# Kernel optimization log

Measured on AMD Instinct MI355X. Metric: run time of the kernel, lower is better.

## Reference

```python
import jax, jax.numpy as jnp
import numpy as np

B, T, C, H, HD = 2, 2048, 1024, 16, 64
EPS = 1e-6

def rmsnorm(x):
    return x * jax.lax.rsqrt(jnp.mean(x * x, axis=-1, keepdims=True) + EPS)

def rotary_cos_sin(seq_len, hd):
    inv_freq = 1.0 / (10000.0 ** (jnp.arange(0, hd, 2, dtype=jnp.float32) / hd))
    freqs = jnp.arange(seq_len, dtype=jnp.float32)[:, None] * inv_freq[None, :]  # [T, hd/2]
    return jnp.cos(freqs)[None, :, None, :], jnp.sin(freqs)[None, :, None, :]

def apply_rotary(x, cos, sin):
    x1, x2 = x[..., : HD // 2], x[..., HD // 2 :]
    return jnp.concatenate([x1 * cos + x2 * sin, -x1 * sin + x2 * cos], axis=-1)


def setup_inputs() -> dict:
    key = jax.random.key(0)
    ks = jax.random.split(key, 8)
    return {
        "x": jax.random.normal(ks[0], (B, T, C), jnp.float32),
        "w_qkv": jax.random.normal(ks[1], (3 * C, C), jnp.float32) * 0.02,
        "w_out": jax.random.normal(ks[2], (C, C), jnp.float32) * 0.02,
        "hyp_curvature": jax.random.uniform(ks[3], (1, H, 1, 1), jnp.float32, 0.5, 1.5),
        "w_uv": jax.random.normal(ks[4], (8 * C, C), jnp.float32) * 0.02,
        "b_uv": jnp.zeros((8 * C,), jnp.float32),
        "w_mlp_out": jax.random.normal(ks[5], (C, 4 * C), jnp.float32) * 0.02,
        "b_mlp_out": jnp.zeros((C,), jnp.float32),
    }


def reference(x, w_qkv, w_out, hyp_curvature, w_uv, b_uv, w_mlp_out, b_mlp_out):
    # --- pre-norm (euc/hyp branch uses rms_norm) ---
    h = rmsnorm(x)
    # --- QKV projection ---
    qkv = h @ w_qkv.T  # [B,T,3C]
    q, k, v = jnp.split(qkv, 3, axis=-1)
    q = q.reshape(B, T, H, HD)
    k = k.reshape(B, T, H, HD)
    v = v.reshape(B, T, H, HD)
    # --- RoPE ---
    cos, sin = rotary_cos_sin(T, HD)
    q = apply_rotary(q, cos, sin)
    k = apply_rotary(k, cos, sin)
    # [B,H,T,HD]
    q = jnp.transpose(q, (0, 2, 1, 3))
    k = jnp.transpose(k, (0, 2, 1, 3))
    v = jnp.transpose(v, (0, 2, 1, 3))
    # --- hyperbolic (Lorentz) attention ---
    kc = hyp_curvature  # [1,H,1,1], positive per-head curvature
    q0 = jnp.sqrt(kc + jnp.sum(q * q, axis=-1, keepdims=True))  # time coord [B,H,T,1]
    k0 = jnp.sqrt(kc + jnp.sum(k * k, axis=-1, keepdims=True))
    # Lorentz inner product <u,v>_L = -u0*v0 + u.v  -> [B,H,T,S]
    lorentz = jnp.einsum("bhtd,bhsd->bhts", q, k) - q0 * jnp.swapaxes(k0, -1, -2)
    dis = jnp.sqrt(kc) * jnp.arccosh(jnp.maximum(-lorentz / kc, 1.0 + EPS))
    causal = jnp.tril(jnp.ones((T, T), dtype=bool))
    scores = jnp.where(causal, -dis, -jnp.inf)  # hyp_attn_weight='neg_dis'
    attn_w = jax.nn.softmax(scores, axis=-1)
    attn = jnp.einsum("bhts,bhsd->bhtd", attn_w, v)
    attn = jnp.transpose(attn, (0, 2, 1, 3)).reshape(B, T, C)
    x = x + attn @ w_out.T
    # --- SwiGLU MLP with pre rms_norm ---
    h = rmsnorm(x)
    uv = h @ w_uv.T + b_uv
    u, vg = jnp.split(uv, 2, axis=-1)
    h_mlp = (u * jax.nn.silu(vg)) @ w_mlp_out.T + b_mlp_out
    return x + h_mlp
```

## Files before the change

kernel.cpp:

```cpp
#include <hip/hip_runtime.h>
#include <cstdint>
#include <cmath>

typedef __bf16 bf16;
typedef __attribute__((ext_vector_type(8))) __bf16 bf16x8;
typedef __attribute__((ext_vector_type(4))) __bf16 bf16x4;
typedef __attribute__((ext_vector_type(2))) __bf16 bf16x2;
typedef __attribute__((ext_vector_type(4))) float f32x4;

constexpr int B_ = 2, T_ = 2048, C_ = 1024, H_ = 16, HD_ = 64;
constexpr int M_ = B_ * T_;

#define EXP2F(x) __builtin_amdgcn_exp2f(x)
#define LOG2F(x) __builtin_amdgcn_logf(x)
#define SQRTF(x) __builtin_amdgcn_sqrtf(x)
#define RCPF(x)  __builtin_amdgcn_rcpf(x)

__device__ __forceinline__ void gld16(const void* g, void* l) {
  __builtin_amdgcn_global_load_lds((const __attribute__((address_space(1))) void*)g,
                                   (__attribute__((address_space(3))) void*)l, 16, 0, 0);
}

__global__ __launch_bounds__(256) void cast_all_kernel(const float* __restrict__ s0,
                                                       const float* __restrict__ s1,
                                                       const float* __restrict__ s2,
                                                       const float* __restrict__ s3,
                                                       const float* __restrict__ s4,
                                                       bf16* __restrict__ d0,
                                                       bf16* __restrict__ d1,
                                                       bf16* __restrict__ d2,
                                                       bf16* __restrict__ d3,
                                                       float* __restrict__ d4) {
  size_t gid = (size_t)blockIdx.x * 256 + threadIdx.x;
  if (gid >= 786432 + 262144 + 2097152 + 1048576) {
    size_t g4 = gid - (786432 + 262144 + 2097152 + 1048576);
    if (g4 >= 2048) return;
    int r = (int)(g4 * 4);
    int dr;
    if (r < 4096) { int blk = r >> 6, i = r & 63; dr = blk * 128 + i; }
    else { int j = r - 4096; int blk = j >> 6, i = j & 63; dr = blk * 128 + 64 + i; }
    *(f32x4*)(d4 + dr) = *(const f32x4*)(s4 + r);
    return;
  }
  const float* src;
  bf16* dst;
  size_t dstoff;
  if (gid < 786432) { src = s0; dst = d0; dstoff = gid * 4; }
  else if (gid < 786432 + 262144) { gid -= 786432; src = s1; dst = d1; dstoff = gid * 4; }
  else if (gid < 786432 + 262144 + 2097152) {
    gid -= 786432 + 262144; src = s2; dst = d2;
    size_t elem = gid * 4;
    int r = (int)(elem >> 10), c = (int)(elem & 1023);
    int dr;
    if (r < 4096) { int blk = r >> 6, i = r & 63; dr = blk * 128 + i; }
    else { int j = r - 4096; int blk = j >> 6, i = j & 63; dr = blk * 128 + 64 + i; }
    dstoff = ((size_t)dr << 10) | (size_t)c;
  }
  else { gid -= 786432 + 262144 + 2097152; src = s3; dst = d3; dstoff = gid * 4; }
  f32x4 v = *(const f32x4*)(src + gid * 4);
  bf16x4 o;
  o[0] = (bf16)v[0]; o[1] = (bf16)v[1]; o[2] = (bf16)v[2]; o[3] = (bf16)v[3];
  *(bf16x4*)(dst + dstoff) = o;
}

template <int MODE, typename OutT, int BM = 128>
__global__ __launch_bounds__(256) void gemm_bt(const bf16* __restrict__ A,
                                               const bf16* __restrict__ Bw,
                                               OutT* __restrict__ Cmat,
                                               const float* __restrict__ bias,
                                               const float* __restrict__ R,
                                               int M, int N, int K, int lda) {
  __shared__ __align__(16) bf16 shmem[(2 * BM + 2 * 128) * 32];
  bf16* const AlsH[2] = { &shmem[0], &shmem[BM * 32] };
  bf16* const BlsH[2] = { &shmem[2 * BM * 32], &shmem[2 * BM * 32 + 4096] };
  const int tid  = threadIdx.x;
  const int wave = tid >> 6;
  const int lane = tid & 63;
  const int quad = lane >> 4;
  const int l16  = lane & 15;
  const int bm = blockIdx.x * BM;
  const int bn = blockIdx.y * 128;
  const int wm = (wave & 1) * (BM / 2);
  const int wn = (wave >> 1) * 64;
  const int wn2 = (wave >> 1) * 32;
  const int srow   = lane >> 2;
  const int schunk = lane & 3;
  constexpr int MT = BM / 32;

  f32x4 acc[MT][4];
#pragma unroll
  for (int i = 0; i < MT; i++)
#pragma unroll
    for (int j = 0; j < 4; j++) acc[i][j] = f32x4{0.f, 0.f, 0.f, 0.f};

  const bf16* Ag = A  + (size_t)(bm + wave * (BM / 4) + srow) * lda + schunk * 8;
  const bf16* Bg = Bw + (size_t)(bn + wave * 32 + srow) * K   + schunk * 8;
  bf16* AlsW0 = AlsH[0] + (wave * (BM / 4)) * 32;
  bf16* AlsW1 = AlsH[1] + (wave * (BM / 4)) * 32;
  bf16* BlsW0 = BlsH[0] + (wave * 32) * 32;
  bf16* BlsW1 = BlsH[1] + (wave * 32) * 32;

  for (int k0 = 0; k0 < K; k0 += 64) {
    gld16(Ag + k0, AlsW0);
    if (BM == 128) gld16(Ag + k0 + (size_t)16 * lda, AlsW0 + 16 * 32);
    gld16(Ag + k0 + 32, AlsW1);
    if (BM == 128) gld16(Ag + k0 + 32 + (size_t)16 * lda, AlsW1 + 16 * 32);
    gld16(Bg + k0,                       BlsW0);
    gld16(Bg + k0 + (size_t)16 * K,      BlsW0 + 16 * 32);
    gld16(Bg + k0 + 32,                  BlsW1);
    gld16(Bg + k0 + 32 + (size_t)16 * K, BlsW1 + 16 * 32);
    __syncthreads();

#pragma unroll
    for (int hh = 0; hh < 2; hh++) {
      bf16x8 af[MT], bfr[4];
#pragma unroll
      for (int mt = 0; mt < MT; mt++)
        af[mt] = *(const bf16x8*)&AlsH[hh][(wm + mt * 16 + l16) * 32 + quad * 8];
#pragma unroll
      for (int nt = 0; nt < 4; nt++) {
        const int cb = (MODE == 4)
                         ? ((nt < 2) ? (wn2 + nt * 16) : (64 + wn2 + (nt - 2) * 16))
                         : (wn + nt * 16);
        bfr[nt] = *(const bf16x8*)&BlsH[hh][(cb + l16) * 32 + quad * 8];
      }
#pragma unroll
      for (int mt = 0; mt < MT; mt++)
#pragma unroll
        for (int nt = 0; nt < 4; nt++)
          acc[mt][nt] = __builtin_amdgcn_mfma_f32_16x16x32_bf16(af[mt], bfr[nt], acc[mt][nt], 0, 0, 0);
    }
    __syncthreads();
  }

  if (MODE != 4) {
#pragma unroll
    for (int mt = 0; mt < MT; mt++) {
      const int row = bm + wm + mt * 16 + quad * 4;
#pragma unroll
      for (int nt = 0; nt < 4; nt++) {
        const int col = bn + wn + nt * 16 + l16;
        float bval = 0.f;
        if (MODE & 2) bval = bias[col];
#pragma unroll
        for (int r = 0; r < 4; r++) {
          float v = acc[mt][nt][r] + bval;
          if (MODE & 1) v += R[(size_t)(row + r) * N + col];
          Cmat[(size_t)(row + r) * N + col] = (OutT)v;
        }
      }
    }
  } else {
    const int colg0 = (bn >> 1) + wn2;
#pragma unroll
    for (int mt = 0; mt < MT; mt++) {
      const int row = bm + wm + mt * 16 + quad * 4;
#pragma unroll
      for (int ntl = 0; ntl < 2; ntl++) {
        const float bu = bias[bn + wn2 + ntl * 16 + l16];
        const float bv = bias[bn + 64 + wn2 + ntl * 16 + l16];
        const int col = colg0 + ntl * 16 + l16;
#pragma unroll
        for (int r = 0; r < 4; r++) {
          float u = acc[mt][ntl][r] + bu;
          float v = acc[mt][ntl + 2][r] + bv;
          float sig = RCPF(1.f + EXP2F(-v * 1.44269504f));
          Cmat[(size_t)(row + r) * N + col] = (OutT)(u * v * sig);
        }
      }
    }
  }
}

__global__ __launch_bounds__(256) void rmsnorm_kernel(const float* __restrict__ X,
                                                      bf16* __restrict__ O) {
  const int row = blockIdx.x;
  const int tid = threadIdx.x;
  const int wave = tid >> 6;
  f32x4 v = *(const f32x4*)(X + (size_t)row * C_ + tid * 4);
  float s = v[0] * v[0] + v[1] * v[1] + v[2] * v[2] + v[3] * v[3];
#pragma unroll
  for (int off = 32; off >= 1; off >>= 1) s += __shfl_xor(s, off);
  __shared__ float wsum[4];
  __shared__ float scale_sh;
  if ((tid & 63) == 0) wsum[wave] = s;
  __syncthreads();
  if (tid == 0)
    scale_sh = rsqrtf((wsum[0] + wsum[1] + wsum[2] + wsum[3]) * (1.f / (float)C_) + 1e-6f);
  __syncthreads();
  const float sc = scale_sh;
  bf16x4 o;
  o[0] = (bf16)(v[0] * sc); o[1] = (bf16)(v[1] * sc);
  o[2] = (bf16)(v[2] * sc); o[3] = (bf16)(v[3] * sc);
  *(bf16x4*)(O + (size_t)row * C_ + tid * 4) = o;
}

__global__ __launch_bounds__(256) void rotary_kernel(bf16* __restrict__ qkv,
                                                     const float* __restrict__ kcb,
                                                     float* __restrict__ q0b,
                                                     float* __restrict__ k0b) {
  const int wid  = blockIdx.x * 4 + (threadIdx.x >> 6);
  const int lane = threadIdx.x & 63;
  const int b = wid >> 15;
  const int rem = wid & 32767;
  const int t = rem >> 4;
  const int h = rem & 15;
  const int i = lane & 31;
  const float invf = expf(-((float)i / 32.f) * 9.210340371976184f);
  const float ang = (float)t * invf;
  const float cx = cosf(ang), sx = sinf(ang);
  const float kc = kcb[h];
  bf16* qp = qkv + (size_t)(b * T_ + t) * 3072 + h * 64;

#pragma unroll
  for (int which = 0; which < 2; which++) {
    bf16* p = qp + which * 1024;
    float x1 = (float)p[i];
    float x2 = (float)p[i + 32];
    float o = (lane < 32) ? (x1 * cx + x2 * sx) : (x2 * cx - x1 * sx);
    float ss = o * o;
#pragma unroll
    for (int off = 32; off >= 1; off >>= 1) ss += __shfl_xor(ss, off);
    p[lane] = (bf16)o;
    if (lane == 0) {
      float* dst = which == 0 ? q0b : k0b;
      dst[(size_t)(b * H_ + h) * T_ + t] = SQRTF(kc + ss);
    }
  }
}

__global__ __launch_bounds__(512) void attn_kernel(const bf16* __restrict__ qkv,
                                                   const float* __restrict__ q0b,
                                                   const float* __restrict__ k0b,
                                                   const float* __restrict__ kcb,
                                                   bf16* __restrict__ outp) {
  __shared__ __align__(16) bf16 Kls[2][64][72];
  __shared__ __align__(16) bf16 Vt[2][64][68];
  __shared__ __align__(16) bf16 Pls[8][16 * 36];
  __shared__ float k0s[2][64];

  const int tid = threadIdx.x;
  const int wave = tid >> 6, lane = tid & 63;
  const int quad = lane >> 4, l16 = lane & 15;
  const int bh = blockIdx.x;
  const int b = bh >> 4, h = bh & 15;

  const float kc = kcb[h];
  const float inv_kc = 1.f / kc;
  const float sqkc = SQRTF(kc);
  const int role = tid >> 8;
  const int st = tid & 255;
  const int sp = st & 31, dq = st >> 5;
  bf16* Pl = Pls[wave];
  const float* q0base = q0b + (size_t)(b * H_ + h) * T_;
  const float* k0base = k0b + (size_t)(b * H_ + h) * T_;

  const int ty = 15 - (int)blockIdx.y;
  const int t0 = ty * 128;
  const int tb = t0 + wave * 16;
  const int nIter = 2 * ty + 2;

  const bf16* qrow = qkv + (size_t)(b * T_ + tb + l16) * 3072 + h * 64;
  bf16x8 aq0 = *(const bf16x8*)(qrow + quad * 8);
  bf16x8 aq1 = *(const bf16x8*)(qrow + 32 + quad * 8);
  float q0r[4];
#pragma unroll
  for (int r = 0; r < 4; r++) q0r[r] = q0base[tb + quad * 4 + r];

  f32x4 o[4];
#pragma unroll
  for (int dt = 0; dt < 4; dt++) o[dt] = f32x4{0.f, 0.f, 0.f, 0.f};
  float lrow[4] = {0.f, 0.f, 0.f, 0.f};

  const bf16* base = qkv + (size_t)b * T_ * 3072 + 1024 + role * 1024 + h * 64 + dq * 8;
  bf16x8 pf_a = *(const bf16x8*)(base + (size_t)(2 * sp) * 3072);
  bf16x8 pf_b = *(const bf16x8*)(base + (size_t)(2 * sp + 1) * 3072);
  float k0v = (tid < 64) ? k0base[tid] : 0.f;

  for (int it = 0; it < nIter; ++it) {
    const int s0 = it * 64;
    const int buf = it & 1;
    if (role == 0) {
      *(bf16x8*)&Kls[buf][2 * sp][dq * 8]     = pf_a;
      *(bf16x8*)&Kls[buf][2 * sp + 1][dq * 8] = pf_b;
    } else {
#pragma unroll
      for (int i2 = 0; i2 < 8; i2++) {
        bf16x2 pr;
        pr[0] = pf_a[i2];
        pr[1] = pf_b[i2];
        *(bf16x2*)&Vt[buf][dq * 8 + i2][2 * sp] = pr;
      }
    }
    if (tid < 64) k0s[buf][tid] = k0v;
    __syncthreads();

    const int s0n = (it + 1 < nIter) ? s0 + 64 : s0;
    pf_a = *(const bf16x8*)(base + (size_t)(s0n + 2 * sp) * 3072);
    pf_b = *(const bf16x8*)(base + (size_t)(s0n + 2 * sp + 1) * 3072);
    if (tid < 64) k0v = k0base[s0n + tid];

    if (s0 <= tb + 15) {
      f32x4 sc[4];
#pragma unroll
      for (int nt = 0; nt < 4; nt++) {
        sc[nt] = f32x4{0.f, 0.f, 0.f, 0.f};
        bf16x8 b0 = *(const bf16x8*)&Kls[buf][nt * 16 + l16][quad * 8];
        bf16x8 b1 = *(const bf16x8*)&Kls[buf][nt * 16 + l16][32 + quad * 8];
        sc[nt] = __builtin_amdgcn_mfma_f32_16x16x32_bf16(aq0, b0, sc[nt], 0, 0, 0);
        sc[nt] = __builtin_amdgcn_mfma_f32_16x16x32_bf16(aq1, b1, sc[nt], 0, 0, 0);
      }

      bf16x8 ap[2];
#pragma unroll
      for (int ck = 0; ck < 2; ck++) {
#pragma unroll
        for (int ntl = 0; ntl < 2; ntl++) {
          const int nt = ck * 2 + ntl;
          const float k0c = k0s[buf][nt * 16 + l16];
          const int s = s0 + nt * 16 + l16;
#pragma unroll
          for (int r = 0; r < 4; r++) {
            const int t = tb + quad * 4 + r;
            float lor = sc[nt][r] - q0r[r] * k0c;
            float ratio = fmaxf(-lor * inv_kc, 1.f + 1e-6f);
            float wv = ratio + SQRTF(ratio * ratio - 1.f);
            float p = EXP2F(-sqkc * LOG2F(wv));
            p = (s <= t) ? p : 0.f;
            lrow[r] += p;
            Pl[(quad * 4 + r) * 36 + ntl * 16 + l16] = (bf16)p;
          }
        }
        ap[ck] = *(const bf16x8*)&Pl[l16 * 36 + quad * 8];
      }
#pragma unroll
      for (int dt = 0; dt < 4; dt++) {
        bf16x8 bv0 = *(const bf16x8*)&Vt[buf][dt * 16 + l16][quad * 8];
        bf16x8 bv1 = *(const bf16x8*)&Vt[buf][dt * 16 + l16][32 + quad * 8];
        o[dt] = __builtin_amdgcn_mfma_f32_16x16x32_bf16(ap[0], bv0, o[dt], 0, 0, 0);
        o[dt] = __builtin_amdgcn_mfma_f32_16x16x32_bf16(ap[1], bv1, o[dt], 0, 0, 0);
      }
    }
  }

#pragma unroll
  for (int r = 0; r < 4; r++) {
#pragma unroll
    for (int off = 1; off <= 8; off <<= 1) lrow[r] += __shfl_xor(lrow[r], off);
  }
#pragma unroll
  for (int r = 0; r < 4; r++) {
    const float invl = RCPF(lrow[r]);
    const int t = tb + quad * 4 + r;
#pragma unroll
    for (int dt = 0; dt < 4; dt++) {
      float val = o[dt][r] * invl;
      outp[(size_t)(b * T_ + t) * C_ + h * 64 + dt * 16 + l16] = (bf16)val;
    }
  }
}

extern "C" void kernel_launch(void* const* d_in, const int* in_sizes, int n_in,
                              void* d_out, int out_size, void* d_ws, size_t ws_size,
                              hipStream_t stream) {
  const float* x      = (const float*)d_in[0];
  const float* w_qkv  = (const float*)d_in[1];
  const float* w_out  = (const float*)d_in[2];
  const float* kcb    = (const float*)d_in[3];
  const float* w_uv   = (const float*)d_in[4];
  const float* b_uv   = (const float*)d_in[5];
  const float* w_mlp  = (const float*)d_in[6];
  const float* b_mlp  = (const float*)d_in[7];
  float* out = (float*)d_out;

  const size_t MB = 1024ull * 1024ull;
  char* w = (char*)d_ws;
  bf16*  wqkv_b  = (bf16*)(w + 0);
  bf16*  wout_b  = (bf16*)(w + 6 * MB);
  bf16*  wuv_p   = (bf16*)(w + 8 * MB);
  bf16*  wmlp_b  = (bf16*)(w + 24 * MB);
  bf16*  hbuf    = (bf16*)(w + 32 * MB);
  bf16*  qkvbuf  = (bf16*)(w + 40 * MB);
  bf16*  attnbuf = (bf16*)(w + 64 * MB);
  bf16*  gbuf    = (bf16*)(w + 40 * MB);
  float* x2buf   = (float*)(w + 72 * MB);
  float* q0b     = (float*)(w + 88 * MB);
  float* k0b     = (float*)(w + 88 * MB + 256 * 1024);
  float* biasp   = (float*)(w + 88 * MB + 512 * 1024);

  const int total4 = 786432 + 262144 + 2097152 + 1048576 + 2048;
  cast_all_kernel<<<(total4 + 255) / 256, 256, 0, stream>>>(
      w_qkv, w_out, w_uv, w_mlp, b_uv, wqkv_b, wout_b, wuv_p, wmlp_b, biasp);

  rmsnorm_kernel<<<M_, 256, 0, stream>>>(x, hbuf);
  gemm_bt<0, bf16><<<dim3(M_ / 128, 3072 / 128), 256, 0, stream>>>(
      hbuf, wqkv_b, qkvbuf, nullptr, nullptr, M_, 3072, 1024, 1024);
  rotary_kernel<<<(B_ * T_ * H_) / 4, 256, 0, stream>>>(qkvbuf, kcb, q0b, k0b);
  attn_kernel<<<dim3(B_ * H_, 16), 512, 0, stream>>>(qkvbuf, q0b, k0b, kcb, attnbuf);
  gemm_bt<1, float, 64><<<dim3(M_ / 64, 1024 / 128), 256, 0, stream>>>(
      attnbuf, wout_b, x2buf, nullptr, x, M_, 1024, 1024, 1024);
  rmsnorm_kernel<<<M_, 256, 0, stream>>>(x2buf, hbuf);
  gemm_bt<4, bf16><<<dim3(M_ / 128, 8192 / 128), 256, 0, stream>>>(
      hbuf, wuv_p, gbuf, biasp, nullptr, M_, 4096, 1024, 1024);
  gemm_bt<3, float, 64><<<dim3(M_ / 64, 1024 / 128), 256, 0, stream>>>(
      gbuf, wmlp_b, out, b_mlp, x2buf, M_, 1024, 4096, 4096);
}
```

Baseline: 416.3 us.

## Fuse rotary and Lorentz time coordinate into QKV GEMM epilogue, merge rmsnorm into cast

```diff
diff --git a/kernel.cpp b/kernel.cpp
--- a/kernel.cpp
+++ b/kernel.cpp
@@ -21,7 +21,8 @@
                                    (__attribute__((address_space(3))) void*)l, 16, 0, 0);
 }
 
-__global__ __launch_bounds__(256) void cast_all_kernel(const float* __restrict__ s0,
+constexpr int CAST_BLOCKS = 16392;
+__global__ __launch_bounds__(256) void cast_rms_kernel(const float* __restrict__ s0,
                                                        const float* __restrict__ s1,
                                                        const float* __restrict__ s2,
                                                        const float* __restrict__ s3,
@@ -30,7 +31,31 @@
                                                        bf16* __restrict__ d1,
                                                        bf16* __restrict__ d2,
                                                        bf16* __restrict__ d3,
-                                                       float* __restrict__ d4) {
+                                                       float* __restrict__ d4,
+                                                       const float* __restrict__ xin,
+                                                       bf16* __restrict__ hout) {
+  if (blockIdx.x >= CAST_BLOCKS) {
+    const int row = blockIdx.x - CAST_BLOCKS;
+    const int tid = threadIdx.x;
+    const int wave = tid >> 6;
+    f32x4 v = *(const f32x4*)(xin + (size_t)row * C_ + tid * 4);
+    float s = v[0] * v[0] + v[1] * v[1] + v[2] * v[2] + v[3] * v[3];
+#pragma unroll
+    for (int off = 32; off >= 1; off >>= 1) s += __shfl_xor(s, off);
+    __shared__ float wsum[4];
+    __shared__ float scale_sh;
+    if ((tid & 63) == 0) wsum[wave] = s;
+    __syncthreads();
+    if (tid == 0)
+      scale_sh = rsqrtf((wsum[0] + wsum[1] + wsum[2] + wsum[3]) * (1.f / (float)C_) + 1e-6f);
+    __syncthreads();
+    const float sc = scale_sh;
+    bf16x4 o;
+    o[0] = (bf16)(v[0] * sc); o[1] = (bf16)(v[1] * sc);
+    o[2] = (bf16)(v[2] * sc); o[3] = (bf16)(v[3] * sc);
+    *(bf16x4*)(hout + (size_t)row * C_ + tid * 4) = o;
+    return;
+  }
   size_t gid = (size_t)blockIdx.x * 256 + threadIdx.x;
   if (gid >= 786432 + 262144 + 2097152 + 1048576) {
     size_t g4 = gid - (786432 + 262144 + 2097152 + 1048576);
@@ -69,6 +94,9 @@
                                                OutT* __restrict__ Cmat,
                                                const float* __restrict__ bias,
                                                const float* __restrict__ R,
+                                               float* __restrict__ q0o,
+                                               float* __restrict__ k0o,
+                                               const float* __restrict__ kcv,
                                                int M, int N, int K, int lda) {
   __shared__ __align__(16) bf16 shmem[(2 * BM + 2 * 128) * 32];
   bf16* const AlsH[2] = { &shmem[0], &shmem[BM * 32] };
@@ -133,24 +161,7 @@
     __syncthreads();
   }
 
-  if (MODE != 4) {
-#pragma unroll
-    for (int mt = 0; mt < MT; mt++) {
-      const int row = bm + wm + mt * 16 + quad * 4;
-#pragma unroll
-      for (int nt = 0; nt < 4; nt++) {
-        const int col = bn + wn + nt * 16 + l16;
-        float bval = 0.f;
-        if (MODE & 2) bval = bias[col];
-#pragma unroll
-        for (int r = 0; r < 4; r++) {
-          float v = acc[mt][nt][r] + bval;
-          if (MODE & 1) v += R[(size_t)(row + r) * N + col];
-          Cmat[(size_t)(row + r) * N + col] = (OutT)v;
-        }
-      }
-    }
-  } else {
+  if (MODE == 4) {
     const int colg0 = (bn >> 1) + wn2;
 #pragma unroll
     for (int mt = 0; mt < MT; mt++) {
@@ -166,6 +177,75 @@
           float v = acc[mt][ntl + 2][r] + bv;
           float sig = RCPF(1.f + EXP2F(-v * 1.44269504f));
           Cmat[(size_t)(row + r) * N + col] = (OutT)(u * v * sig);
+        }
+      }
+    }
+  } else if (MODE == 5) {
+    const int cbase = bn + wn;
+    if (cbase < 2048) {
+      const bool isq = cbase < 1024;
+      const int h = (isq ? cbase : cbase - 1024) >> 6;
+      const float kc = kcv[h];
+      float invf[2];
+#pragma unroll
+      for (int ntl = 0; ntl < 2; ntl++)
+        invf[ntl] = EXP2F(-((float)(ntl * 16 + l16) / 32.f) * 13.287712379549449f);
+#pragma unroll
+      for (int mt = 0; mt < MT; mt++) {
+        float ssl[4] = {0.f, 0.f, 0.f, 0.f};
+#pragma unroll
+        for (int ntl = 0; ntl < 2; ntl++) {
+#pragma unroll
+          for (int r = 0; r < 4; r++) {
+            const int row = bm + wm + mt * 16 + quad * 4 + r;
+            const float ang = (float)(row & 2047) * invf[ntl];
+            const float c = cosf(ang), s = sinf(ang);
+            const float x1 = acc[mt][ntl][r];
+            const float x2 = acc[mt][ntl + 2][r];
+            const float o1 = x1 * c + x2 * s;
+            const float o2 = x2 * c - x1 * s;
+            acc[mt][ntl][r] = o1;
+            acc[mt][ntl + 2][r] = o2;
+            ssl[r] += o1 * o1 + o2 * o2;
+          }
+        }
+#pragma unroll
+        for (int r = 0; r < 4; r++) {
+#pragma unroll
+          for (int off = 1; off <= 8; off <<= 1) ssl[r] += __shfl_xor(ssl[r], off);
+          if (l16 == 0) {
+            const int row = bm + wm + mt * 16 + quad * 4 + r;
+            float* dst = isq ? q0o : k0o;
+            dst[((size_t)((row >> 11) * 16 + h)) * 2048 + (row & 2047)] = SQRTF(kc + ssl[r]);
+          }
+        }
+      }
+    }
+#pragma unroll
+    for (int mt = 0; mt < MT; mt++) {
+      const int row = bm + wm + mt * 16 + quad * 4;
+#pragma unroll
+      for (int nt = 0; nt < 4; nt++) {
+        const int col = bn + wn + nt * 16 + l16;
+#pragma unroll
+        for (int r = 0; r < 4; r++)
+          Cmat[(size_t)(row + r) * N + col] = (OutT)acc[mt][nt][r];
+      }
+    }
+  } else {
+#pragma unroll
+    for (int mt = 0; mt < MT; mt++) {
+      const int row = bm + wm + mt * 16 + quad * 4;
+#pragma unroll
+      for (int nt = 0; nt < 4; nt++) {
+        const int col = bn + wn + nt * 16 + l16;
+        float bval = 0.f;
+        if (MODE & 2) bval = bias[col];
+#pragma unroll
+        for (int r = 0; r < 4; r++) {
+          float v = acc[mt][nt][r] + bval;
+          if (MODE & 1) v += R[(size_t)(row + r) * N + col];
+          Cmat[(size_t)(row + r) * N + col] = (OutT)v;
         }
       }
     }
@@ -193,40 +273,6 @@
   o[0] = (bf16)(v[0] * sc); o[1] = (bf16)(v[1] * sc);
   o[2] = (bf16)(v[2] * sc); o[3] = (bf16)(v[3] * sc);
   *(bf16x4*)(O + (size_t)row * C_ + tid * 4) = o;
-}
-
-__global__ __launch_bounds__(256) void rotary_kernel(bf16* __restrict__ qkv,
-                                                     const float* __restrict__ kcb,
-                                                     float* __restrict__ q0b,
-                                                     float* __restrict__ k0b) {
-  const int wid  = blockIdx.x * 4 + (threadIdx.x >> 6);
-  const int lane = threadIdx.x & 63;
-  const int b = wid >> 15;
-  const int rem = wid & 32767;
-  const int t = rem >> 4;
-  const int h = rem & 15;
-  const int i = lane & 31;
-  const float invf = expf(-((float)i / 32.f) * 9.210340371976184f);
-  const float ang = (float)t * invf;
-  const float cx = cosf(ang), sx = sinf(ang);
-  const float kc = kcb[h];
-  bf16* qp = qkv + (size_t)(b * T_ + t) * 3072 + h * 64;
-
-#pragma unroll
-  for (int which = 0; which < 2; which++) {
-    bf16* p = qp + which * 1024;
-    float x1 = (float)p[i];
-    float x2 = (float)p[i + 32];
-    float o = (lane < 32) ? (x1 * cx + x2 * sx) : (x2 * cx - x1 * sx);
-    float ss = o * o;
-#pragma unroll
-    for (int off = 32; off >= 1; off >>= 1) ss += __shfl_xor(ss, off);
-    p[lane] = (bf16)o;
-    if (lane == 0) {
-      float* dst = which == 0 ? q0b : k0b;
-      dst[(size_t)(b * H_ + h) * T_ + t] = SQRTF(kc + ss);
-    }
-  }
 }
 
 __global__ __launch_bounds__(512) void attn_kernel(const bf16* __restrict__ qkv,
@@ -388,20 +434,17 @@
   float* k0b     = (float*)(w + 88 * MB + 256 * 1024);
   float* biasp   = (float*)(w + 88 * MB + 512 * 1024);
 
-  const int total4 = 786432 + 262144 + 2097152 + 1048576 + 2048;
-  cast_all_kernel<<<(total4 + 255) / 256, 256, 0, stream>>>(
-      w_qkv, w_out, w_uv, w_mlp, b_uv, wqkv_b, wout_b, wuv_p, wmlp_b, biasp);
-
-  rmsnorm_kernel<<<M_, 256, 0, stream>>>(x, hbuf);
-  gemm_bt<0, bf16><<<dim3(M_ / 128, 3072 / 128), 256, 0, stream>>>(
-      hbuf, wqkv_b, qkvbuf, nullptr, nullptr, M_, 3072, 1024, 1024);
-  rotary_kernel<<<(B_ * T_ * H_) / 4, 256, 0, stream>>>(qkvbuf, kcb, q0b, k0b);
+  cast_rms_kernel<<<CAST_BLOCKS + M_, 256, 0, stream>>>(
+      w_qkv, w_out, w_uv, w_mlp, b_uv, wqkv_b, wout_b, wuv_p, wmlp_b, biasp, x, hbuf);
+
+  gemm_bt<5, bf16><<<dim3(M_ / 128, 3072 / 128), 256, 0, stream>>>(
+      hbuf, wqkv_b, qkvbuf, nullptr, nullptr, q0b, k0b, kcb, M_, 3072, 1024, 1024);
   attn_kernel<<<dim3(B_ * H_, 16), 512, 0, stream>>>(qkvbuf, q0b, k0b, kcb, attnbuf);
   gemm_bt<1, float, 64><<<dim3(M_ / 64, 1024 / 128), 256, 0, stream>>>(
-      attnbuf, wout_b, x2buf, nullptr, x, M_, 1024, 1024, 1024);
+      attnbuf, wout_b, x2buf, nullptr, x, nullptr, nullptr, nullptr, M_, 1024, 1024, 1024);
   rmsnorm_kernel<<<M_, 256, 0, stream>>>(x2buf, hbuf);
   gemm_bt<4, bf16><<<dim3(M_ / 128, 8192 / 128), 256, 0, stream>>>(
-      hbuf, wuv_p, gbuf, biasp, nullptr, M_, 4096, 1024, 1024);
+      hbuf, wuv_p, gbuf, biasp, nullptr, nullptr, nullptr, nullptr, M_, 4096, 1024, 1024);
   gemm_bt<3, float, 64><<<dim3(M_ / 64, 1024 / 128), 256, 0, stream>>>(
-      gbuf, wmlp_b, out, b_mlp, x2buf, M_, 1024, 4096, 4096);
-}
+      gbuf, wmlp_b, out, b_mlp, x2buf, nullptr, nullptr, nullptr, M_, 1024, 4096, 4096);
+}
```

New measurement: 670.4 us. 61.0% more time.
